# Optimization experiments

Hardware: AMD Instinct MI355X
Metric: run time of the kernel (lower is better)

## Reference

```python
import jax, jax.numpy as jnp
import numpy as np

HEADS = 8
TOPK = 32
LN_EPS = 1e-5


def _ln(x, g, b):
    m = jnp.mean(x, axis=-1, keepdims=True)
    v = jnp.var(x, axis=-1, keepdims=True)
    return (x - m) * jax.lax.rsqrt(v + LN_EPS) * g + b


def _split_heads(t):
    B, N, I = t.shape
    return t.reshape(B, N, HEADS, I // HEADS).transpose(0, 2, 1, 3)


def _merge_heads(t):
    B, H, N, D = t.shape
    return t.transpose(0, 2, 1, 3).reshape(B, N, H * D)


def _mha(xq, xkv, wq, wk, wv, wo, bo):
    # standard softmax cross-attention (SDPA branch, topk<=0), scale=1/sqrt(d_head)
    q = _split_heads(xq @ wq)
    k = _split_heads(xkv @ wk)
    v = _split_heads(xkv @ wv)
    scale = q.shape[-1] ** -0.5
    attn = jax.nn.softmax(jnp.einsum('bhnd,bhmd->bhnm', q, k) * scale, axis=-1)
    o = jnp.einsum('bhnm,bhmd->bhnd', attn, v)
    return _merge_heads(o) @ wo + bo


def _topk_attn(x, wq, wk, wv, wo, bo):
    # top-k sparse self-attention branch: softmax over the k largest logits per query,
    # all other attention weights are exactly zero -> equivalent to gathering the
    # selected value rows and contracting (avoids materializing the scattered matrix).
    q = _split_heads(x @ wq)
    k = _split_heads(x @ wk)
    v = _split_heads(x @ wv)
    scale = q.shape[-1] ** -0.5
    dots = jnp.einsum('bhnd,bhmd->bhnm', q, k) * scale  # [B,H,N,N]
    top_dots, top_inds = jax.lax.top_k(dots, TOPK)      # [B,H,N,K]
    top_attn = jax.nn.softmax(top_dots, axis=-1)
    # v_sel[b,h,n,k,d] = v[b,h,top_inds[b,h,n,k],d]
    v_sel = jnp.take_along_axis(v[:, :, None, :, :], top_inds[..., None], axis=3)
    o = jnp.einsum('bhnk,bhnkd->bhnd', top_attn, v_sel)
    return _merge_heads(o) @ wo + bo


def _geglu_ff(x, w1, b1, w2, b2):
    h = x @ w1 + b1
    a, g = jnp.split(h, 2, axis=-1)
    return (a * jax.nn.gelu(g, approximate=False)) @ w2 + b2


def _forward(x, context,
             ctx_wq, ctx_wk, ctx_wv, ctx_wo, ctx_bo, cn_g, cn_b,
             im_wq, im_wk, im_wv, im_wo, im_bo,
             xc_wq, xc_wk, xc_wv, xc_wo, xc_bo,
             ffc_w1, ffc_b1, ffc_w2, ffc_b2,
             ffi_w1, ffi_b1, ffi_w2, ffi_b2,
             n1_g, n1_b, n2_g, n2_b, n3_g, n3_b):
    # context self-attention (nx_enhanced=1) + context feed-forward
    cn = _ln(context, cn_g, cn_b)
    c = context + _mha(cn, cn, ctx_wq, ctx_wk, ctx_wv, ctx_wo, ctx_bo)
    c = c + _geglu_ff(c, ffc_w1, ffc_b1, ffc_w2, ffc_b2)
    # image-token top-k sparse self-attention
    h = x + _topk_attn(_ln(x, n1_g, n1_b), im_wq, im_wk, im_wv, im_wo, im_bo)
    # image -> context cross-attention
    h = h + _mha(_ln(h, n2_g, n2_b), c, xc_wq, xc_wk, xc_wv, xc_wo, xc_bo)
    # image feed-forward (GEGLU)
    h = h + _geglu_ff(_ln(h, n3_g, n3_b), ffi_w1, ffi_b1, ffi_w2, ffi_b2)
    return h


def setup_inputs() -> dict:
    key = jax.random.key(0)
    ki = iter(jax.random.split(key, 64))
    def w(*shape):
        return jax.random.normal(next(ki), shape, jnp.float32) * 0.02
    C, D, I = 768, 512, 512
    inp = dict(
        x=jax.random.normal(next(ki), (2, 2304, D), jnp.float32),
        context=jax.random.normal(next(ki), (2, 256, C), jnp.float32),
        spatial_shapes=jnp.array([[48, 48]], dtype=jnp.int32),  # 48*48 == 2304
        ctx_wq=w(C, I), ctx_wk=w(C, I), ctx_wv=w(C, I), ctx_wo=w(I, C),
        ctx_bo=jnp.zeros((C,), jnp.float32),
        cn_g=jnp.ones((C,), jnp.float32), cn_b=jnp.zeros((C,), jnp.float32),
        im_wq=w(D, I), im_wk=w(D, I), im_wv=w(D, I), im_wo=w(I, D),
        im_bo=jnp.zeros((D,), jnp.float32),
        xc_wq=w(D, I), xc_wk=w(C, I), xc_wv=w(C, I), xc_wo=w(I, D),
        xc_bo=jnp.zeros((D,), jnp.float32),
        ffc_w1=w(C, 8 * C), ffc_b1=jnp.zeros((8 * C,), jnp.float32),
        ffc_w2=w(4 * C, C), ffc_b2=jnp.zeros((C,), jnp.float32),
        ffi_w1=w(D, 8 * D), ffi_b1=jnp.zeros((8 * D,), jnp.float32),
        ffi_w2=w(4 * D, D), ffi_b2=jnp.zeros((D,), jnp.float32),
        n1_g=jnp.ones((D,), jnp.float32), n1_b=jnp.zeros((D,), jnp.float32),
        n2_g=jnp.ones((D,), jnp.float32), n2_b=jnp.zeros((D,), jnp.float32),
        n3_g=jnp.ones((D,), jnp.float32), n3_b=jnp.zeros((D,), jnp.float32),
    )
    return inp


def reference(x, context, spatial_shapes,
              ctx_wq, ctx_wk, ctx_wv, ctx_wo, ctx_bo, cn_g, cn_b,
              im_wq, im_wk, im_wv, im_wo, im_bo,
              xc_wq, xc_wk, xc_wv, xc_wo, xc_bo,
              ffc_w1, ffc_b1, ffc_w2, ffc_b2,
              ffi_w1, ffi_b1, ffi_w2, ffi_b2,
              n1_g, n1_b, n2_g, n2_b, n3_g, n3_b):
    del spatial_shapes  # only consumed by the (disabled) deformable path
    return _forward(x, context,
                    ctx_wq, ctx_wk, ctx_wv, ctx_wo, ctx_bo, cn_g, cn_b,
                    im_wq, im_wk, im_wv, im_wo, im_bo,
                    xc_wq, xc_wk, xc_wv, xc_wo, xc_bo,
                    ffc_w1, ffc_b1, ffc_w2, ffc_b2,
                    ffi_w1, ffi_b1, ffi_w2, ffi_b2,
                    n1_g, n1_b, n2_g, n2_b, n3_g, n3_b)
```

## Files before the change

### kernel.cpp

```cpp
#include <hip/hip_runtime.h>
#include <hip/hip_bf16.h>
#include <hip/hip_fp16.h>
#include <cmath>

typedef unsigned short u16;
typedef unsigned long long ull;
typedef __attribute__((ext_vector_type(8))) short short8;
typedef __attribute__((ext_vector_type(4))) float f32x4;
typedef __attribute__((ext_vector_type(4))) unsigned short u16x4;

__device__ __forceinline__ u16 f2bf(float x) {
    unsigned u = __float_as_uint(x);
    u += 0x7fffu + ((u >> 16) & 1u);
    return (u16)(u >> 16);
}
__device__ __forceinline__ float bf2f(u16 b) {
    return __uint_as_float(((unsigned)b) << 16);
}

__device__ __forceinline__ unsigned h2key(unsigned hb) {
    return (hb & 0x8000u) ? (hb ^ 0xFFFFu) : (hb | 0x8000u);
}
__device__ __forceinline__ float key2f(unsigned k) {
    unsigned hb = (k & 0x8000u) ? (k ^ 0x8000u) : (k ^ 0xFFFFu);
    return __half2float(__ushort_as_half((unsigned short)hb));
}

typedef __attribute__((address_space(3))) unsigned int as3_uint;
typedef __attribute__((address_space(1))) unsigned int as1_uint;
__device__ __forceinline__ void gload_lds16(const u16* g, u16* l) {
    __builtin_amdgcn_global_load_lds(
        (as1_uint*)(unsigned long long)(const void*)g,
        (as3_uint*)(unsigned int)(unsigned long long)(const void*)l,
        16, 0, 0);
}

__device__ __forceinline__ float gelu_exact(float g) {
    return 0.5f * g * (1.f + erff(g * 0.70710678118654752f));
}

struct TBatch {
    const float* src[16];
    u16* dst[16];
    int K[16];
    int N[16];
    int start[17];
};

__global__ void k_transpose_cast_batch(TBatch tb) {
    __shared__ float tile[32][33];
    int t = blockIdx.x;
    int m = 0;
    while (t >= tb.start[m + 1]) ++m;
    int rel = t - tb.start[m];
    const int K = tb.K[m], N = tb.N[m];
    const int ntx = N >> 5;
    const int n0 = (rel % ntx) * 32, k0 = (rel / ntx) * 32;
    const float* __restrict__ in = tb.src[m];
    u16* __restrict__ out = tb.dst[m];
    int tx = threadIdx.x, ty = threadIdx.y;
#pragma unroll
    for (int j = 0; j < 4; ++j)
        tile[ty + j * 8][tx] = in[(size_t)(k0 + ty + j * 8) * N + n0 + tx];
    __syncthreads();
#pragma unroll
    for (int j = 0; j < 4; ++j)
        out[(size_t)(n0 + ty + j * 8) * K + k0 + tx] = f2bf(tile[tx][ty + j * 8]);
}

__global__ void k_vtrans16(const u16* __restrict__ in, int stride, int coloff,
                           u16* __restrict__ out) {
    __shared__ int tile[32][33];
    int tx = threadIdx.x, ty = threadIdx.y;
    int d0 = blockIdx.x * 32, k0 = blockIdx.y * 32, b = blockIdx.z;
#pragma unroll
    for (int j = 0; j < 4; ++j)
        tile[ty + j * 8][tx] = in[(size_t)(b * 256 + k0 + ty + j * 8) * stride + coloff + d0 + tx];
    __syncthreads();
#pragma unroll
    for (int j = 0; j < 4; ++j)
        out[(size_t)(b * 512 + d0 + ty + j * 8) * 256 + k0 + tx] = (u16)tile[tx][ty + j * 8];
}

__global__ __launch_bounds__(256)
void k_ln_bf16(const float* __restrict__ in, const float* __restrict__ gam,
               const float* __restrict__ bet, u16* __restrict__ out, int F) {
    int lane = threadIdx.x & 63, w = threadIdx.x >> 6;
    int row = blockIdx.x * 4 + w;
    const int F4 = F >> 2;
    const float4* r4 = reinterpret_cast<const float4*>(in + (size_t)row * F);
    const float4* g4 = reinterpret_cast<const float4*>(gam);
    const float4* b4 = reinterpret_cast<const float4*>(bet);
    float s = 0.f, s2 = 0.f;
    for (int j = lane; j < F4; j += 64) {
        float4 v = r4[j];
        s += v.x + v.y + v.z + v.w;
        s2 += v.x * v.x + v.y * v.y + v.z * v.z + v.w * v.w;
    }
#pragma unroll
    for (int off = 32; off; off >>= 1) { s += __shfl_xor(s, off); s2 += __shfl_xor(s2, off); }
    float mean = s / F;
    float var  = s2 / F - mean * mean;
    float inv  = 1.f / sqrtf(var + 1e-5f);
    u16x4* o4 = reinterpret_cast<u16x4*>(out + (size_t)row * F);
    for (int j = lane; j < F4; j += 64) {
        float4 v = r4[j], gm = g4[j], bt = b4[j];
        u16x4 o;
        o[0] = f2bf((v.x - mean) * inv * gm.x + bt.x);
        o[1] = f2bf((v.y - mean) * inv * gm.y + bt.y);
        o[2] = f2bf((v.z - mean) * inv * gm.z + bt.z);
        o[3] = f2bf((v.w - mean) * inv * gm.w + bt.w);
        o4[j] = o;
    }
}

template <int BM, int BN>
__global__ __launch_bounds__(256)
void gemm_bt(const u16* __restrict__ A, const u16* __restrict__ Bt,
             const float* __restrict__ bias, const float* __restrict__ res,
             float* __restrict__ out32, u16* __restrict__ out16,
             int M, int N, int K) {
    constexpr int WM = BM / 2, WN = BN / 2, FM = WM / 16, FN = WN / 16;
    __shared__ __align__(16) u16 As[BM * 32];
    __shared__ __align__(16) u16 Bs[BN * 32];
    const int tid = threadIdx.x;
    const int lane = tid & 63;
    const int wid = tid >> 6;
    const int wr = wid >> 1, wc = wid & 1;
    const int nwg = gridDim.x * gridDim.y;
    int lin = blockIdx.y * gridDim.x + blockIdx.x;
    lin = (lin & 7) * (nwg >> 3) + (lin >> 3);
    const int m0 = (lin / gridDim.x) * BM, n0 = (lin % gridDim.x) * BN;
    const int r16 = lane & 15;
    const int g8  = (lane >> 4) * 8;
    const int w16 = wid * 16;
    const int ln4 = lane >> 2;
    const int cb8 = (lane & 3) * 8;

    const f32x4 zero4 = {0.f, 0.f, 0.f, 0.f};
    f32x4 acc[FM][FN];
#pragma unroll
    for (int m = 0; m < FM; ++m)
#pragma unroll
        for (int n = 0; n < FN; ++n) acc[m][n] = zero4;

    for (int k0 = 0; k0 < K; k0 += 32) {
#pragma unroll
        for (int p = 0; p < BM / 64; ++p) {
            const int rb = p * 64 + w16;
            gload_lds16(A + (size_t)(m0 + rb + ln4) * K + k0 + cb8, &As[rb * 32]);
        }
#pragma unroll
        for (int p = 0; p < BN / 64; ++p) {
            const int rb = p * 64 + w16;
            gload_lds16(Bt + (size_t)(n0 + rb + ln4) * K + k0 + cb8, &Bs[rb * 32]);
        }
        __syncthreads();
        short8 af[FM], bfr[FN];
#pragma unroll
        for (int m = 0; m < FM; ++m)
            af[m] = *reinterpret_cast<const short8*>(&As[(wr * WM + m * 16 + r16) * 32 + g8]);
#pragma unroll
        for (int n = 0; n < FN; ++n)
            bfr[n] = *reinterpret_cast<const short8*>(&Bs[(wc * WN + n * 16 + r16) * 32 + g8]);
#pragma unroll
        for (int m = 0; m < FM; ++m)
#pragma unroll
            for (int n = 0; n < FN; ++n)
                acc[m][n] = __builtin_amdgcn_mfma_f32_16x16x32_bf16(af[m], bfr[n], acc[m][n], 0, 0, 0);
        __syncthreads();
    }

    const int rg = (lane >> 4) * 4;
#pragma unroll
    for (int m = 0; m < FM; ++m) {
#pragma unroll
        for (int n = 0; n < FN; ++n) {
#pragma unroll
            for (int j = 0; j < 4; ++j) {
                int row = m0 + wr * WM + m * 16 + rg + j;
                int col = n0 + wc * WN + n * 16 + r16;
                float v = acc[m][n][j];
                if (bias) v += bias[col];
                size_t off = (size_t)row * N + col;
                if (res) v += res[off];
                if (out32) out32[off] = v;
                if (out16) out16[off] = f2bf(v);
            }
        }
    }
}

template <int BM>
__global__ __launch_bounds__(256)
void gemm_geglu(const u16* __restrict__ A, const u16* __restrict__ Bt,
                const float* __restrict__ bias, u16* __restrict__ out16,
                int M, int Nh, int K) {
    constexpr int WM = BM / 2, FM = WM / 16;
    __shared__ __align__(16) u16 As[BM * 32];
    __shared__ __align__(16) u16 Bs[128 * 32];
    const int tid = threadIdx.x;
    const int lane = tid & 63;
    const int wid = tid >> 6;
    const int wr = wid >> 1, wc = wid & 1;
    const int nwg = gridDim.x * gridDim.y;
    int lin = blockIdx.y * gridDim.x + blockIdx.x;
    lin = (lin & 7) * (nwg >> 3) + (lin >> 3);
    const int m0 = (lin / gridDim.x) * BM, n0 = (lin % gridDim.x) * 64;
    const int r16 = lane & 15;
    const int g8  = (lane >> 4) * 8;
    const int w16 = wid * 16;
    const int ln4 = lane >> 2;
    const int cb8 = (lane & 3) * 8;

    const f32x4 zero4 = {0.f, 0.f, 0.f, 0.f};
    f32x4 acc_a[FM][2], acc_g[FM][2];
#pragma unroll
    for (int m = 0; m < FM; ++m)
#pragma unroll
        for (int n = 0; n < 2; ++n) { acc_a[m][n] = zero4; acc_g[m][n] = zero4; }

    for (int k0 = 0; k0 < K; k0 += 32) {
#pragma unroll
        for (int p = 0; p < BM / 64; ++p) {
            const int rb = p * 64 + w16;
            gload_lds16(A + (size_t)(m0 + rb + ln4) * K + k0 + cb8, &As[rb * 32]);
        }
        gload_lds16(Bt + (size_t)(n0 + w16 + ln4) * K + k0 + cb8, &Bs[w16 * 32]);
        gload_lds16(Bt + (size_t)(Nh + n0 + w16 + ln4) * K + k0 + cb8, &Bs[(64 + w16) * 32]);
        __syncthreads();
        short8 af[FM], ba[2], bg[2];
#pragma unroll
        for (int m = 0; m < FM; ++m)
            af[m] = *reinterpret_cast<const short8*>(&As[(wr * WM + m * 16 + r16) * 32 + g8]);
#pragma unroll
        for (int n = 0; n < 2; ++n) {
            ba[n] = *reinterpret_cast<const short8*>(&Bs[(wc * 32 + n * 16 + r16) * 32 + g8]);
            bg[n] = *reinterpret_cast<const short8*>(&Bs[(64 + wc * 32 + n * 16 + r16) * 32 + g8]);
        }
#pragma unroll
        for (int m = 0; m < FM; ++m)
#pragma unroll
            for (int n = 0; n < 2; ++n) {
                acc_a[m][n] = __builtin_amdgcn_mfma_f32_16x16x32_bf16(af[m], ba[n], acc_a[m][n], 0, 0, 0);
                acc_g[m][n] = __builtin_amdgcn_mfma_f32_16x16x32_bf16(af[m], bg[n], acc_g[m][n], 0, 0, 0);
            }
        __syncthreads();
    }

    const int rg = (lane >> 4) * 4;
#pragma unroll
    for (int m = 0; m < FM; ++m) {
#pragma unroll
        for (int n = 0; n < 2; ++n) {
#pragma unroll
            for (int j = 0; j < 4; ++j) {
                int row = m0 + wr * WM + m * 16 + rg + j;
                int col = n0 + wc * 32 + n * 16 + r16;
                float a = acc_a[m][n][j] + bias[col];
                float g = acc_g[m][n][j] + bias[Nh + col];
                out16[(size_t)row * Nh + col] = f2bf(a * gelu_exact(g));
            }
        }
    }
}

__global__ __launch_bounds__(256)
void k_attn_mfma(const u16* __restrict__ Qb, int sq, const u16* __restrict__ Kb,
                 int sk, const u16* __restrict__ VT, u16* __restrict__ out, int NQ) {
    __shared__ float sc[16][268];
    __shared__ u16   pb[16][268];
    const int tid = threadIdx.x, lane = tid & 63, w = tid >> 6;
    const int nqb = NQ >> 4;
    const int h = blockIdx.x & 7;
    const int rest = blockIdx.x >> 3;
    const int b = rest / nqb;
    const int q0 = (rest % nqb) << 4;
    const int r16 = lane & 15, g8 = (lane >> 4) * 8, rq = (lane >> 4) * 4;

    const size_t qrow = ((size_t)(b * NQ + q0 + r16)) * sq + h * 64;
    const short8 af0 = *reinterpret_cast<const short8*>(Qb + qrow + g8);
    const short8 af1 = *reinterpret_cast<const short8*>(Qb + qrow + 32 + g8);
    const u16* kb = Kb + (size_t)b * 256 * sk + h * 64;
    const f32x4 zero4 = {0.f, 0.f, 0.f, 0.f};
#pragma unroll
    for (int t = 0; t < 4; ++t) {
        const size_t krow = (size_t)(t * 64 + w * 16 + r16) * sk;
        const short8 bf0 = *reinterpret_cast<const short8*>(kb + krow + g8);
        const short8 bf1 = *reinterpret_cast<const short8*>(kb + krow + 32 + g8);
        f32x4 acc = __builtin_amdgcn_mfma_f32_16x16x32_bf16(af0, bf0, zero4, 0, 0, 0);
        acc = __builtin_amdgcn_mfma_f32_16x16x32_bf16(af1, bf1, acc, 0, 0, 0);
        const int col = t * 64 + w * 16 + r16;
#pragma unroll
        for (int j = 0; j < 4; ++j) sc[rq + j][col] = acc[j] * 0.125f;
    }
    __syncthreads();
#pragma unroll
    for (int qi = 0; qi < 4; ++qi) {
        const int q = w * 4 + qi;
        float4 v = *reinterpret_cast<const float4*>(&sc[q][lane * 4]);
        float m = fmaxf(fmaxf(v.x, v.y), fmaxf(v.z, v.w));
#pragma unroll
        for (int off = 32; off; off >>= 1) m = fmaxf(m, __shfl_xor(m, off));
        float e0 = expf(v.x - m), e1 = expf(v.y - m), e2 = expf(v.z - m), e3 = expf(v.w - m);
        float sum = e0 + e1 + e2 + e3;
#pragma unroll
        for (int off = 32; off; off >>= 1) sum += __shfl_xor(sum, off);
        float inv = 1.f / sum;
        u16x4 p4;
        p4[0] = f2bf(e0 * inv); p4[1] = f2bf(e1 * inv);
        p4[2] = f2bf(e2 * inv); p4[3] = f2bf(e3 * inv);
        *reinterpret_cast<u16x4*>(&pb[q][lane * 4]) = p4;
    }
    __syncthreads();
    f32x4 o = zero4;
    const u16* vt = VT + ((size_t)(b * 512 + h * 64 + w * 16 + r16)) * 256;
#pragma unroll
    for (int kk = 0; kk < 8; ++kk) {
        const short8 pa = *reinterpret_cast<const short8*>(&pb[r16][kk * 32 + g8]);
        const short8 vv = *reinterpret_cast<const short8*>(vt + kk * 32 + g8);
        o = __builtin_amdgcn_mfma_f32_16x16x32_bf16(pa, vv, o, 0, 0, 0);
    }
#pragma unroll
    for (int j = 0; j < 4; ++j)
        out[((size_t)(b * NQ + q0 + rq + j)) * 512 + h * 64 + w * 16 + r16] = f2bf(o[j]);
}

__global__ __launch_bounds__(256)
void gemm_scores(const u16* __restrict__ QKV, u16* __restrict__ keys) {
    __shared__ __align__(16) u16 As[2][128 * 32];
    __shared__ __align__(16) u16 Bs[2][128 * 32];
    const int tid = threadIdx.x;
    const int lane = tid & 63;
    const int wid = tid >> 6;
    const int wr = wid >> 1, wc = wid & 1;
    int lin = blockIdx.x;
    lin = (lin & 7) * 648 + (lin >> 3);
    const int bh = lin / 324;
    const int rel = lin % 324;
    const int m0 = (rel / 18) * 128, n0 = (rel % 18) * 128;
    const int b = bh >> 3, h = bh & 7;
    const u16* Qb = QKV + (size_t)b * 2304 * 1536 + h * 64;
    const u16* Kb = Qb + 512;
    const int r16 = lane & 15;
    const int g8  = (lane >> 4) * 8;
    const int w16 = wid * 16;
    const int ln4 = lane >> 2;
    const int cb8 = (lane & 3) * 8;

#pragma unroll
    for (int kk = 0; kk < 2; ++kk) {
#pragma unroll
        for (int p = 0; p < 2; ++p) {
            const int rb = p * 64 + w16;
            gload_lds16(Qb + (size_t)(m0 + rb + ln4) * 1536 + kk * 32 + cb8, &As[kk][rb * 32]);
            gload_lds16(Kb + (size_t)(n0 + rb + ln4) * 1536 + kk * 32 + cb8, &Bs[kk][rb * 32]);
        }
    }
    __syncthreads();

    const f32x4 zero4 = {0.f, 0.f, 0.f, 0.f};
    f32x4 acc[4][4];
#pragma unroll
    for (int m = 0; m < 4; ++m)
#pragma unroll
        for (int n = 0; n < 4; ++n) acc[m][n] = zero4;

    short8 af[2][4], bfr[2][4];
#pragma unroll
    for (int kk = 0; kk < 2; ++kk)
#pragma unroll
        for (int m = 0; m < 4; ++m) {
            af[kk][m] = *reinterpret_cast<const short8*>(&As[kk][(wr * 64 + m * 16 + r16) * 32 + g8]);
            bfr[kk][m] = *reinterpret_cast<const short8*>(&Bs[kk][(wc * 64 + m * 16 + r16) * 32 + g8]);
        }
#pragma unroll
    for (int kk = 0; kk < 2; ++kk)
#pragma unroll
        for (int m = 0; m < 4; ++m)
#pragma unroll
            for (int n = 0; n < 4; ++n)
                acc[m][n] = __builtin_amdgcn_mfma_f32_16x16x32_bf16(af[kk][m], bfr[kk][n], acc[m][n], 0, 0, 0);

    u16* kout = keys + (size_t)bh * 2304 * 2304;
    const int rg = (lane >> 4) * 4;
#pragma unroll
    for (int m = 0; m < 4; ++m) {
#pragma unroll
        for (int n = 0; n < 4; ++n) {
#pragma unroll
            for (int j = 0; j < 4; ++j) {
                int row = m0 + wr * 64 + m * 16 + rg + j;
                int col = n0 + wc * 64 + n * 16 + r16;
                unsigned hb = __half_as_ushort(__float2half(acc[m][n][j] * 0.125f));
                kout[(size_t)row * 2304 + col] = (u16)h2key(hb);
            }
        }
    }
}

__global__ __launch_bounds__(256)
void k_topk_sel(const u16* __restrict__ keys, const u16* __restrict__ QKV,
                u16* __restrict__ out) {
    __shared__ int   ilist[4][32];
    __shared__ float wlist[4][32];
    const int tid = threadIdx.x, lane = tid & 63, w = tid >> 6;
    const int h = blockIdx.x & 7;
    const int t7 = blockIdx.x >> 3;
    const int b = t7 / 576;
    const int q = (t7 % 576) * 4 + w;

    const u16* krow = keys + ((size_t)((b * 8 + h) * 2304) + q) * 2304;
    const ull ltm = (1ull << lane) - 1ull;
    unsigned key[36];
#pragma unroll
    for (int j = 0; j < 36; ++j)
        key[j] = krow[lane + j * 64];

    unsigned thr = 0;
    for (int bit = 15; bit >= 0; --bit) {
        const unsigned cand = thr | (1u << bit);
        int c = 0, done = 0;
#pragma unroll
        for (int blk = 0; blk < 6; ++blk) {
            if (!done) {
#pragma unroll
                for (int u = 0; u < 6; ++u)
                    c += (int)__popcll(__ballot(key[blk * 6 + u] >= cand));
                if (c >= 32) done = 1;
            }
        }
        if (c >= 32) thr = cand;
    }
    int tot = 0;
#pragma unroll
    for (int j = 0; j < 36; ++j) {
        bool p = key[j] > thr;
        ull m = __ballot(p);
        if (p) {
            int pos = tot + (int)__popcll(m & ltm);
            ilist[w][pos] = j * 64 + lane;
            wlist[w][pos] = key2f(key[j]);
        }
        tot += (int)__popcll(m);
    }
    const int r = 32 - tot;
    const float tv = key2f(thr);
    int t2 = 0;
#pragma unroll
    for (int j = 0; j < 36; ++j) {
        bool p = (key[j] == thr);
        ull m = __ballot(p);
        if (p) {
            int pos = t2 + (int)__popcll(m & ltm);
            if (pos < r) { ilist[w][tot + pos] = j * 64 + lane; wlist[w][tot + pos] = tv; }
        }
        t2 += (int)__popcll(m);
    }
    float wv = (lane < 32) ? wlist[w][lane] : -3.0e38f;
    float mf = wv;
#pragma unroll
    for (int off = 32; off; off >>= 1) mf = fmaxf(mf, __shfl_xor(mf, off));
    float e = (lane < 32) ? expf(wv - mf) : 0.f;
    float sum = e;
#pragma unroll
    for (int off = 32; off; off >>= 1) sum += __shfl_xor(sum, off);
    if (lane < 32) wlist[w][lane] = e / sum;
    const u16* vb = QKV + (size_t)b * 2304 * 1536 + 1024 + h * 64 + lane;
    u16 vr[32];
#pragma unroll
    for (int i = 0; i < 32; ++i)
        vr[i] = vb[(size_t)ilist[w][i] * 1536];
    float o = 0.f;
#pragma unroll
    for (int i = 0; i < 32; ++i)
        o += wlist[w][i] * bf2f(vr[i]);
    out[((size_t)(b * 2304 + q)) * 512 + h * 64 + lane] = f2bf(o);
}

static constexpr size_t O_WQKVC = 0;
static constexpr size_t O_WOC   = O_WQKVC + 2359296;
static constexpr size_t O_W1C   = O_WOC + 786432;
static constexpr size_t O_W2C   = O_W1C + 9437184;
static constexpr size_t O_WQKVI = O_W2C + 4718592;
static constexpr size_t O_WOI   = O_WQKVI + 1572864;
static constexpr size_t O_WQX   = O_WOI + 524288;
static constexpr size_t O_WKVX  = O_WQX + 524288;
static constexpr size_t O_WOX   = O_WKVX + 1572864;
static constexpr size_t O_W1I   = O_WOX + 524288;
static constexpr size_t O_W2I   = O_W1I + 4194304;
static constexpr size_t O_CF16  = O_W2I + 2097152;
static constexpr size_t O_H     = O_CF16 + 786432;
static constexpr size_t O_H2    = O_H + 9437184;
static constexpr size_t O_S     = O_H2 + 9437184;
static constexpr size_t O_CN16  = O_S;
static constexpr size_t O_QKVC  = O_CN16 + 786432;
static constexpr size_t O_VTC   = O_QKVC + 1572864;
static constexpr size_t O_AO16  = O_VTC + 524288;
static constexpr size_t O_CBUF  = O_AO16 + 524288;
static constexpr size_t O_C16   = O_CBUF + 1572864;
static constexpr size_t O_AG16  = O_C16 + 786432;
static constexpr size_t O_XLN   = O_S;
static constexpr size_t O_QKVI  = O_XLN + 4718592;
static constexpr size_t O_KEYS  = O_QKVI + 14155776;
static constexpr size_t O_TO16  = O_KEYS + 169869312;
static constexpr size_t O_H2LN  = O_S;
static constexpr size_t O_XQ    = O_H2LN + 4718592;
static constexpr size_t O_KVX   = O_XQ + 4718592;
static constexpr size_t O_VTX   = O_KVX + 1048576;
static constexpr size_t O_XO16  = O_VTX + 524288;
static constexpr size_t O_H3    = O_S;
static constexpr size_t O_AGI   = O_H3 + 4718592;

extern "C" void kernel_launch(void* const* d_in, const int* in_sizes, int n_in,
                              void* d_out, int out_size, void* d_ws, size_t ws_size,
                              hipStream_t stream) {
    (void)in_sizes; (void)n_in; (void)out_size; (void)ws_size;
    const float* x      = (const float*)d_in[0];
    const float* ctx    = (const float*)d_in[1];
    const float* ctx_wq = (const float*)d_in[3];
    const float* ctx_wk = (const float*)d_in[4];
    const float* ctx_wv = (const float*)d_in[5];
    const float* ctx_wo = (const float*)d_in[6];
    const float* ctx_bo = (const float*)d_in[7];
    const float* cn_g   = (const float*)d_in[8];
    const float* cn_b   = (const float*)d_in[9];
    const float* im_wq  = (const float*)d_in[10];
    const float* im_wk  = (const float*)d_in[11];
    const float* im_wv  = (const float*)d_in[12];
    const float* im_wo  = (const float*)d_in[13];
    const float* im_bo  = (const float*)d_in[14];
    const float* xc_wq  = (const float*)d_in[15];
    const float* xc_wk  = (const float*)d_in[16];
    const float* xc_wv  = (const float*)d_in[17];
    const float* xc_wo  = (const float*)d_in[18];
    const float* xc_bo  = (const float*)d_in[19];
    const float* ffc_w1 = (const float*)d_in[20];
    const float* ffc_b1 = (const float*)d_in[21];
    const float* ffc_w2 = (const float*)d_in[22];
    const float* ffc_b2 = (const float*)d_in[23];
    const float* ffi_w1 = (const float*)d_in[24];
    const float* ffi_b1 = (const float*)d_in[25];
    const float* ffi_w2 = (const float*)d_in[26];
    const float* ffi_b2 = (const float*)d_in[27];
    const float* n1_g   = (const float*)d_in[28];
    const float* n1_b   = (const float*)d_in[29];
    const float* n2_g   = (const float*)d_in[30];
    const float* n2_b   = (const float*)d_in[31];
    const float* n3_g   = (const float*)d_in[32];
    const float* n3_b   = (const float*)d_in[33];
    char* ws = (char*)d_ws;
    float* out = (float*)d_out;
    auto Wp = [&](size_t off) { return (u16*)(ws + off); };
    auto Fp = [&](size_t off) { return (float*)(ws + off); };
    dim3 tb(32, 8);

    TBatch tbat;
    const float* srcs[16] = {ctx_wq, ctx_wk, ctx_wv, ctx_wo, ffc_w1, ffc_w2,
                             im_wq, im_wk, im_wv, im_wo, xc_wq, xc_wk, xc_wv,
                             xc_wo, ffi_w1, ffi_w2};
    const size_t dsts[16] = {O_WQKVC, O_WQKVC + 786432, O_WQKVC + 1572864, O_WOC,
                             O_W1C, O_W2C,
                             O_WQKVI, O_WQKVI + 524288, O_WQKVI + 1048576, O_WOI,
                             O_WQX, O_WKVX, O_WKVX + 786432, O_WOX,
                             O_W1I, O_W2I};
    const int Ks[16] = {768, 768, 768, 512, 768, 3072, 512, 512, 512, 512,
                        512, 768, 768, 512, 512, 2048};
    const int Ns[16] = {512, 512, 512, 768, 6144, 768, 512, 512, 512, 512,
                        512, 512, 512, 512, 4096, 512};
    int acc = 0;
    for (int i = 0; i < 16; ++i) {
        tbat.src[i] = srcs[i];
        tbat.dst[i] = Wp(dsts[i]);
        tbat.K[i] = Ks[i];
        tbat.N[i] = Ns[i];
        tbat.start[i] = acc;
        acc += (Ns[i] >> 5) * (Ks[i] >> 5);
    }
    tbat.start[16] = acc;
    k_transpose_cast_batch<<<acc, tb, 0, stream>>>(tbat);

    k_ln_bf16<<<128, 256, 0, stream>>>(ctx, cn_g, cn_b, Wp(O_CN16), 768);
    gemm_bt<64, 64><<<dim3(24, 8), 256, 0, stream>>>(Wp(O_CN16), Wp(O_WQKVC), nullptr, nullptr, nullptr, Wp(O_QKVC), 512, 1536, 768);
    k_vtrans16<<<dim3(16, 8, 2), tb, 0, stream>>>(Wp(O_QKVC), 1536, 1024, Wp(O_VTC));
    k_attn_mfma<<<256, 256, 0, stream>>>(Wp(O_QKVC), 1536, Wp(O_QKVC) + 512, 1536, Wp(O_VTC), Wp(O_AO16), 256);
    gemm_bt<64, 64><<<dim3(12, 8), 256, 0, stream>>>(Wp(O_AO16), Wp(O_WOC), ctx_bo, ctx, Fp(O_CBUF), Wp(O_C16), 512, 768, 512);
    gemm_geglu<128><<<dim3(48, 4), 256, 0, stream>>>(Wp(O_C16), Wp(O_W1C), ffc_b1, Wp(O_AG16), 512, 3072, 768);
    gemm_bt<64, 64><<<dim3(12, 8), 256, 0, stream>>>(Wp(O_AG16), Wp(O_W2C), ffc_b2, Fp(O_CBUF), nullptr, Wp(O_CF16), 512, 768, 3072);

    k_ln_bf16<<<1152, 256, 0, stream>>>(x, n1_g, n1_b, Wp(O_XLN), 512);
    gemm_bt<128, 128><<<dim3(12, 36), 256, 0, stream>>>(Wp(O_XLN), Wp(O_WQKVI), nullptr, nullptr, nullptr, Wp(O_QKVI), 4608, 1536, 512);
    gemm_scores<<<5184, 256, 0, stream>>>(Wp(O_QKVI), Wp(O_KEYS));
    k_topk_sel<<<9216, 256, 0, stream>>>(Wp(O_KEYS), Wp(O_QKVI), Wp(O_TO16));
    gemm_bt<128, 64><<<dim3(8, 36), 256, 0, stream>>>(Wp(O_TO16), Wp(O_WOI), im_bo, x, Fp(O_H), nullptr, 4608, 512, 512);

    k_ln_bf16<<<1152, 256, 0, stream>>>(Fp(O_H), n2_g, n2_b, Wp(O_H2LN), 512);
    gemm_bt<128, 64><<<dim3(8, 36), 256, 0, stream>>>(Wp(O_H2LN), Wp(O_WQX), nullptr, nullptr, nullptr, Wp(O_XQ), 4608, 512, 512);
    gemm_bt<64, 64><<<dim3(16, 8), 256, 0, stream>>>(Wp(O_CF16), Wp(O_WKVX), nullptr, nullptr, nullptr, Wp(O_KVX), 512, 1024, 768);
    k_vtrans16<<<dim3(16, 8, 2), tb, 0, stream>>>(Wp(O_KVX), 1024, 512, Wp(O_VTX));
    k_attn_mfma<<<2304, 256, 0, stream>>>(Wp(O_XQ), 512, Wp(O_KVX), 1024, Wp(O_VTX), Wp(O_XO16), 2304);
    gemm_bt<128, 64><<<dim3(8, 36), 256, 0, stream>>>(Wp(O_XO16), Wp(O_WOX), xc_bo, Fp(O_H), Fp(O_H2), nullptr, 4608, 512, 512);

    k_ln_bf16<<<1152, 256, 0, stream>>>(Fp(O_H2), n3_g, n3_b, Wp(O_H3), 512);
    gemm_geglu<128><<<dim3(32, 36), 256, 0, stream>>>(Wp(O_H3), Wp(O_W1I), ffi_b1, Wp(O_AGI), 4608, 2048, 512);
    gemm_bt<128, 64><<<dim3(8, 36), 256, 0, stream>>>(Wp(O_AGI), Wp(O_W2I), ffi_b2, Fp(O_H2), out, nullptr, 4608, 512, 2048);
}
```

Baseline: 498.7 us.

## Rework top-k selection with packed 16-bit counting and retune GEMM tiles

The top-k selection kernel now handles two query rows per wavefront. It loads keys as packed 16-bit pairs with vector loads and counts candidates using packed subtract/min instructions instead of per-element ballots. A per-lane max pre-pass narrows the radix search so it can start below the top bit and stop early, and the tail uses LDS atomics to place selected entries. Separately, several GEMM launches move to smaller 64x64 tiles with more blocks, trading per-block reuse for more parallelism. The atomic placement also changes the order of selected indices, which can alter floating-point summation order.

```diff
diff --git a/kernel.cpp b/kernel.cpp
--- a/kernel.cpp
+++ b/kernel.cpp
@@ -399,83 +399,204 @@
     }
 }
 
+#define SEL_TAIL(KP, THR, QIDX, SLOT)                                           \
+    {                                                                           \
+        const unsigned tp = (THR) * 0x10001u;                                   \
+        _Pragma("unroll")                                                       \
+        for (int i = 0; i < 18; ++i) {                                          \
+            unsigned s;                                                         \
+            asm("v_pk_sub_u16 %0, %1, %2 clamp" : "=v"(s) : "v"(KP[i]), "v"(tp)); \
+            if (s) {                                                            \
+                const unsigned klo = KP[i] & 0xFFFFu, khi = KP[i] >> 16;        \
+                const int gbase = (i >> 1) * 256 + lane * 4 + (i & 1) * 2;      \
+                if (klo > (THR)) {                                              \
+                    unsigned pos = atomicAdd(&cnt[SLOT], 1u);                   \
+                    ilist[SLOT][pos] = gbase; wlist[SLOT][pos] = key2f(klo);    \
+                }                                                               \
+                if (khi > (THR)) {                                              \
+                    unsigned pos = atomicAdd(&cnt[SLOT], 1u);                   \
+                    ilist[SLOT][pos] = gbase + 1; wlist[SLOT][pos] = key2f(khi); \
+                }                                                               \
+            }                                                                   \
+        }                                                                       \
+        const int tot = (int)cnt[SLOT];                                         \
+        const int r = 32 - tot;                                                 \
+        if (r > 0) {                                                            \
+            const float tv = key2f(THR);                                        \
+            int t2 = 0;                                                         \
+            _Pragma("unroll")                                                   \
+            for (int j = 0; j < 9; ++j) {                                       \
+                if (t2 < r) {                                                   \
+                    const unsigned x = KP[2 * j], y = KP[2 * j + 1];            \
+                    const unsigned ka = x & 0xFFFFu, kb2 = x >> 16;             \
+                    const unsigned kc = y & 0xFFFFu, kd = y >> 16;              \
+                    const ull e0 = __ballot(ka == (THR));                       \
+                    const ull e1 = __ballot(kb2 == (THR));                      \
+                    const ull e2 = __ballot(kc == (THR));                       \
+                    const ull e3 = __ballot(kd == (THR));                       \
+                    const int base = (int)__popcll(e0 & ltm) + (int)__popcll(e1 & ltm) + \
+                                     (int)__popcll(e2 & ltm) + (int)__popcll(e3 & ltm); \
+                    const int b0 = (int)((e0 >> lane) & 1ull);                  \
+                    const int b1 = b0 + (int)((e1 >> lane) & 1ull);             \
+                    const int b2 = b1 + (int)((e2 >> lane) & 1ull);             \
+                    if (ka == (THR)) { int pos = t2 + base;                     \
+                        if (pos < r) { ilist[SLOT][tot + pos] = j * 256 + lane * 4 + 0; wlist[SLOT][tot + pos] = tv; } } \
+                    if (kb2 == (THR)) { int pos = t2 + base + b0;               \
+                        if (pos < r) { ilist[SLOT][tot + pos] = j * 256 + lane * 4 + 1; wlist[SLOT][tot + pos] = tv; } } \
+                    if (kc == (THR)) { int pos = t2 + base + b1;                \
+                        if (pos < r) { ilist[SLOT][tot + pos] = j * 256 + lane * 4 + 2; wlist[SLOT][tot + pos] = tv; } } \
+                    if (kd == (THR)) { int pos = t2 + base + b2;                \
+                        if (pos < r) { ilist[SLOT][tot + pos] = j * 256 + lane * 4 + 3; wlist[SLOT][tot + pos] = tv; } } \
+                    t2 += (int)__popcll(e0) + (int)__popcll(e1) +               \
+                          (int)__popcll(e2) + (int)__popcll(e3);                \
+                }                                                               \
+            }                                                                   \
+        }                                                                       \
+        float wv = (lane < 32) ? wlist[SLOT][lane] : -3.0e38f;                  \
+        float mf = wv;                                                          \
+        _Pragma("unroll")                                                       \
+        for (int off = 32; off; off >>= 1) mf = fmaxf(mf, __shfl_xor(mf, off)); \
+        float e = (lane < 32) ? expf(wv - mf) : 0.f;                            \
+        float sum = e;                                                          \
+        _Pragma("unroll")                                                       \
+        for (int off = 32; off; off >>= 1) sum += __shfl_xor(sum, off);         \
+        if (lane < 32) wlist[SLOT][lane] = e / sum;                             \
+        const u16* vb = QKV + (size_t)b * 2304 * 1536 + 1024 + h * 64 + lane;   \
+        u16 vr[32];                                                             \
+        _Pragma("unroll")                                                       \
+        for (int i = 0; i < 32; ++i)                                            \
+            vr[i] = vb[(size_t)ilist[SLOT][i] * 1536];                          \
+        float o = 0.f;                                                          \
+        _Pragma("unroll")                                                       \
+        for (int i = 0; i < 32; ++i)                                            \
+            o += wlist[SLOT][i] * bf2f(vr[i]);                                  \
+        out[((size_t)(b * 2304 + (QIDX))) * 512 + h * 64 + lane] = f2bf(o);     \
+    }
+
+#define SEL_PASS(KP, THR, BIT, DONE)                                            \
+    {                                                                           \
+        const unsigned cand = (THR) | (1u << (BIT));                            \
+        const unsigned cm1 = (cand - 1) * 0x10001u;                             \
+        unsigned cacc = 0;                                                      \
+        _Pragma("unroll")                                                       \
+        for (int j = 0; j < 18; ++j) {                                          \
+            unsigned s, m;                                                      \
+            asm("v_pk_sub_u16 %0, %1, %2 clamp" : "=v"(s) : "v"(KP[j]), "v"(cm1)); \
+            asm("v_pk_min_u16 %0, %1, %2" : "=v"(m) : "v"(s), "v"(ones));       \
+            cacc += m;                                                          \
+        }                                                                       \
+        unsigned c = (cacc & 0xFFFFu) + (cacc >> 16);                           \
+        _Pragma("unroll")                                                       \
+        for (int off = 32; off; off >>= 1) c += (unsigned)__shfl_xor((int)c, off); \
+        if (c >= 32) { (THR) = cand; if (c == 32) (DONE) = 1; }                 \
+        if (--(BIT) < 0) (DONE) = 1;                                            \
+    }
+
 __global__ __launch_bounds__(256)
 void k_topk_sel(const u16* __restrict__ keys, const u16* __restrict__ QKV,
                 u16* __restrict__ out) {
-    __shared__ int   ilist[4][32];
-    __shared__ float wlist[4][32];
+    __shared__ int      ilist[8][32];
+    __shared__ float    wlist[8][32];
+    __shared__ unsigned cnt[8];
     const int tid = threadIdx.x, lane = tid & 63, w = tid >> 6;
     const int h = blockIdx.x & 7;
     const int t7 = blockIdx.x >> 3;
-    const int b = t7 / 576;
-    const int q = (t7 % 576) * 4 + w;
-
-    const u16* krow = keys + ((size_t)((b * 8 + h) * 2304) + q) * 2304;
+    const int b = t7 / 288;
+    const int q0 = (t7 % 288) * 8;
+    const int qA = q0 + w * 2, qB = qA + 1;
+    const int sA = w * 2, sB = sA + 1;
+
+    const u16* krowA = keys + ((size_t)((b * 8 + h) * 2304) + qA) * 2304;
+    const u16* krowB = krowA + 2304;
     const ull ltm = (1ull << lane) - 1ull;
-    unsigned key[36];
-#pragma unroll
-    for (int j = 0; j < 36; ++j)
-        key[j] = krow[lane + j * 64];
-
-    unsigned thr = 0;
+    unsigned kpA[18], kpB[18];
+#pragma unroll
+    for (int j = 0; j < 9; ++j) {
+        const uint2 vA = *reinterpret_cast<const uint2*>(krowA + j * 256 + lane * 4);
+        const uint2 vB = *reinterpret_cast<const uint2*>(krowB + j * 256 + lane * 4);
+        kpA[2 * j] = vA.x; kpA[2 * j + 1] = vA.y;
+        kpB[2 * j] = vB.x; kpB[2 * j + 1] = vB.y;
+    }
+    if (lane == 0) { cnt[sA] = 0u; cnt[sB] = 0u; }
+
+    unsigned pmA = kpA[0], pmB = kpB[0];
+#pragma unroll
+    for (int j = 1; j < 18; ++j) {
+        asm("v_pk_max_u16 %0, %1, %2" : "=v"(pmA) : "v"(pmA), "v"(kpA[j]));
+        asm("v_pk_max_u16 %0, %1, %2" : "=v"(pmB) : "v"(pmB), "v"(kpB[j]));
+    }
+    unsigned lmaxA = pmA >> 16, lmaxB = pmB >> 16;
+    {
+        const unsigned loA = pmA & 0xFFFFu, loB = pmB & 0xFFFFu;
+        lmaxA = loA > lmaxA ? loA : lmaxA;
+        lmaxB = loB > lmaxB ? loB : lmaxB;
+    }
+    unsigned m1A = lmaxA, m1B = lmaxB;
+#pragma unroll
+    for (int off = 32; off; off >>= 1) {
+        unsigned oA = (unsigned)__shfl_xor((int)m1A, off);
+        unsigned oB = (unsigned)__shfl_xor((int)m1B, off);
+        m1A = oA > m1A ? oA : m1A;
+        m1B = oB > m1B ? oB : m1B;
+    }
+    unsigned lo32A = 0, lo32B = 0;
+#pragma unroll
     for (int bit = 15; bit >= 0; --bit) {
-        const unsigned cand = thr | (1u << bit);
-        int c = 0, done = 0;
-#pragma unroll
-        for (int blk = 0; blk < 6; ++blk) {
-            if (!done) {
-#pragma unroll
-                for (int u = 0; u < 6; ++u)
-                    c += (int)__popcll(__ballot(key[blk * 6 + u] >= cand));
-                if (c >= 32) done = 1;
-            }
-        }
-        if (c >= 32) thr = cand;
-    }
-    int tot = 0;
-#pragma unroll
-    for (int j = 0; j < 36; ++j) {
-        bool p = key[j] > thr;
-        ull m = __ballot(p);
-        if (p) {
-            int pos = tot + (int)__popcll(m & ltm);
-            ilist[w][pos] = j * 64 + lane;
-            wlist[w][pos] = key2f(key[j]);
-        }
-        tot += (int)__popcll(m);
-    }
-    const int r = 32 - tot;
-    const float tv = key2f(thr);
-    int t2 = 0;
-#pragma unroll
-    for (int j = 0; j < 36; ++j) {
-        bool p = (key[j] == thr);
-        ull m = __ballot(p);
-        if (p) {
-            int pos = t2 + (int)__popcll(m & ltm);
-            if (pos < r) { ilist[w][tot + pos] = j * 64 + lane; wlist[w][tot + pos] = tv; }
-        }
-        t2 += (int)__popcll(m);
-    }
-    float wv = (lane < 32) ? wlist[w][lane] : -3.0e38f;
-    float mf = wv;
-#pragma unroll
-    for (int off = 32; off; off >>= 1) mf = fmaxf(mf, __shfl_xor(mf, off));
-    float e = (lane < 32) ? expf(wv - mf) : 0.f;
-    float sum = e;
-#pragma unroll
-    for (int off = 32; off; off >>= 1) sum += __shfl_xor(sum, off);
-    if (lane < 32) wlist[w][lane] = e / sum;
-    const u16* vb = QKV + (size_t)b * 2304 * 1536 + 1024 + h * 64 + lane;
-    u16 vr[32];
-#pragma unroll
-    for (int i = 0; i < 32; ++i)
-        vr[i] = vb[(size_t)ilist[w][i] * 1536];
-    float o = 0.f;
-#pragma unroll
-    for (int i = 0; i < 32; ++i)
-        o += wlist[w][i] * bf2f(vr[i]);
-    out[((size_t)(b * 2304 + q)) * 512 + h * 64 + lane] = f2bf(o);
+        const unsigned cA = lo32A | (1u << bit);
+        const unsigned cB = lo32B | (1u << bit);
+        const int nA = (int)__popcll(__ballot(lmaxA >= cA));
+        const int nB = (int)__popcll(__ballot(lmaxB >= cB));
+        if (nA >= 32) lo32A = cA;
+        if (nB >= 32) lo32B = cB;
+    }
+
+    const unsigned ones = 0x00010001u;
+    unsigned thrA, thrB;
+    int bitA = -1, bitB = -1, doneA = 0, doneB = 0;
+    if (m1A == lo32A) { thrA = m1A; doneA = 1; }
+    else {
+        const int hb = 31 - __clz(m1A ^ lo32A);
+        thrA = m1A & ~((2u << hb) - 1u);
+        bitA = hb;
+    }
+    if (m1B == lo32B) { thrB = m1B; doneB = 1; }
+    else {
+        const int hb = 31 - __clz(m1B ^ lo32B);
+        thrB = m1B & ~((2u << hb) - 1u);
+        bitB = hb;
+    }
+    while (!doneA && !doneB) {
+        const unsigned candA = thrA | (1u << bitA);
+        const unsigned candB = thrB | (1u << bitB);
+        const unsigned cm1A = (candA - 1) * 0x10001u;
+        const unsigned cm1B = (candB - 1) * 0x10001u;
+        unsigned accA = 0, accB = 0;
+#pragma unroll
+        for (int j = 0; j < 18; ++j) {
+            unsigned sa, ma, sb, mb;
+            asm("v_pk_sub_u16 %0, %1, %2 clamp" : "=v"(sa) : "v"(kpA[j]), "v"(cm1A));
+            asm("v_pk_sub_u16 %0, %1, %2 clamp" : "=v"(sb) : "v"(kpB[j]), "v"(cm1B));
+            asm("v_pk_min_u16 %0, %1, %2" : "=v"(ma) : "v"(sa), "v"(ones));
+            asm("v_pk_min_u16 %0, %1, %2" : "=v"(mb) : "v"(sb), "v"(ones));
+            accA += ma; accB += mb;
+        }
+        unsigned cA = (accA & 0xFFFFu) + (accA >> 16);
+        unsigned cB = (accB & 0xFFFFu) + (accB >> 16);
+#pragma unroll
+        for (int off = 32; off; off >>= 1) {
+            cA += (unsigned)__shfl_xor((int)cA, off);
+            cB += (unsigned)__shfl_xor((int)cB, off);
+        }
+        if (cA >= 32) { thrA = candA; if (cA == 32) doneA = 1; }
+        if (--bitA < 0) doneA = 1;
+        if (cB >= 32) { thrB = candB; if (cB == 32) doneB = 1; }
+        if (--bitB < 0) doneB = 1;
+    }
+    while (!doneA) SEL_PASS(kpA, thrA, bitA, doneA);
+    while (!doneB) SEL_PASS(kpB, thrB, bitB, doneB);
+
+    SEL_TAIL(kpA, thrA, qA, sA);
+    SEL_TAIL(kpB, thrB, qB, sB);
 }
 
 static constexpr size_t O_WQKVC = 0;
@@ -585,23 +706,23 @@
     k_vtrans16<<<dim3(16, 8, 2), tb, 0, stream>>>(Wp(O_QKVC), 1536, 1024, Wp(O_VTC));
     k_attn_mfma<<<256, 256, 0, stream>>>(Wp(O_QKVC), 1536, Wp(O_QKVC) + 512, 1536, Wp(O_VTC), Wp(O_AO16), 256);
     gemm_bt<64, 64><<<dim3(12, 8), 256, 0, stream>>>(Wp(O_AO16), Wp(O_WOC), ctx_bo, ctx, Fp(O_CBUF), Wp(O_C16), 512, 768, 512);
-    gemm_geglu<128><<<dim3(48, 4), 256, 0, stream>>>(Wp(O_C16), Wp(O_W1C), ffc_b1, Wp(O_AG16), 512, 3072, 768);
+    gemm_geglu<64><<<dim3(48, 8), 256, 0, stream>>>(Wp(O_C16), Wp(O_W1C), ffc_b1, Wp(O_AG16), 512, 3072, 768);
     gemm_bt<64, 64><<<dim3(12, 8), 256, 0, stream>>>(Wp(O_AG16), Wp(O_W2C), ffc_b2, Fp(O_CBUF), nullptr, Wp(O_CF16), 512, 768, 3072);
 
     k_ln_bf16<<<1152, 256, 0, stream>>>(x, n1_g, n1_b, Wp(O_XLN), 512);
-    gemm_bt<128, 128><<<dim3(12, 36), 256, 0, stream>>>(Wp(O_XLN), Wp(O_WQKVI), nullptr, nullptr, nullptr, Wp(O_QKVI), 4608, 1536, 512);
+    gemm_bt<64, 64><<<dim3(24, 72), 256, 0, stream>>>(Wp(O_XLN), Wp(O_WQKVI), nullptr, nullptr, nullptr, Wp(O_QKVI), 4608, 1536, 512);
     gemm_scores<<<5184, 256, 0, stream>>>(Wp(O_QKVI), Wp(O_KEYS));
-    k_topk_sel<<<9216, 256, 0, stream>>>(Wp(O_KEYS), Wp(O_QKVI), Wp(O_TO16));
-    gemm_bt<128, 64><<<dim3(8, 36), 256, 0, stream>>>(Wp(O_TO16), Wp(O_WOI), im_bo, x, Fp(O_H), nullptr, 4608, 512, 512);
+    k_topk_sel<<<4608, 256, 0, stream>>>(Wp(O_KEYS), Wp(O_QKVI), Wp(O_TO16));
+    gemm_bt<64, 64><<<dim3(8, 72), 256, 0, stream>>>(Wp(O_TO16), Wp(O_WOI), im_bo, x, Fp(O_H), nullptr, 4608, 512, 512);
 
     k_ln_bf16<<<1152, 256, 0, stream>>>(Fp(O_H), n2_g, n2_b, Wp(O_H2LN), 512);
-    gemm_bt<128, 64><<<dim3(8, 36), 256, 0, stream>>>(Wp(O_H2LN), Wp(O_WQX), nullptr, nullptr, nullptr, Wp(O_XQ), 4608, 512, 512);
+    gemm_bt<64, 64><<<dim3(8, 72), 256, 0, stream>>>(Wp(O_H2LN), Wp(O_WQX), nullptr, nullptr, nullptr, Wp(O_XQ), 4608, 512, 512);
     gemm_bt<64, 64><<<dim3(16, 8), 256, 0, stream>>>(Wp(O_CF16), Wp(O_WKVX), nullptr, nullptr, nullptr, Wp(O_KVX), 512, 1024, 768);
     k_vtrans16<<<dim3(16, 8, 2), tb, 0, stream>>>(Wp(O_KVX), 1024, 512, Wp(O_VTX));
     k_attn_mfma<<<2304, 256, 0, stream>>>(Wp(O_XQ), 512, Wp(O_KVX), 1024, Wp(O_VTX), Wp(O_XO16), 2304);
-    gemm_bt<128, 64><<<dim3(8, 36), 256, 0, stream>>>(Wp(O_XO16), Wp(O_WOX), xc_bo, Fp(O_H), Fp(O_H2), nullptr, 4608, 512, 512);
+    gemm_bt<64, 64><<<dim3(8, 72), 256, 0, stream>>>(Wp(O_XO16), Wp(O_WOX), xc_bo, Fp(O_H), Fp(O_H2), nullptr, 4608, 512, 512);
 
     k_ln_bf16<<<1152, 256, 0, stream>>>(Fp(O_H2), n3_g, n3_b, Wp(O_H3), 512);
     gemm_geglu<128><<<dim3(32, 36), 256, 0, stream>>>(Wp(O_H3), Wp(O_W1I), ffi_b1, Wp(O_AGI), 4608, 2048, 512);
-    gemm_bt<128, 64><<<dim3(8, 36), 256, 0, stream>>>(Wp(O_AGI), Wp(O_W2I), ffi_b2, Fp(O_H2), out, nullptr, 4608, 512, 2048);
-}
+    gemm_bt<64, 64><<<dim3(8, 72), 256, 0, stream>>>(Wp(O_AGI), Wp(O_W2I), ffi_b2, Fp(O_H2), out, nullptr, 4608, 512, 2048);
+}
```

Measured after the change: 433.7 us. -13.0%, faster.
